# Kernel optimization log

Hardware: AMD Instinct MI355X
Metric: run time of the kernel (lower is better)

## Reference

```python
import jax, jax.numpy as jnp
import numpy as np

B, S, D = 2, 2048, 4096
H, KVH, HD = 32, 8, 128          # n_heads, n_kv_heads, head_dim
N_REP = H // KVH                 # GQA repeat factor
ROPE_THETA = 10000.0
NEG = -1e9                       # finite stand-in for -inf additive mask


def setup_inputs() -> dict:
    key = jax.random.key(0)
    ks = jax.random.split(key, 5)
    x = jax.random.normal(ks[0], (B, S, D), jnp.float32)
    wq = jax.random.normal(ks[1], (D, H * HD), jnp.float32) * 0.02
    wk = jax.random.normal(ks[2], (D, KVH * HD), jnp.float32) * 0.02
    wv = jax.random.normal(ks[3], (D, KVH * HD), jnp.float32) * 0.02
    wo = jax.random.normal(ks[4], (D, D), jnp.float32) * 0.02
    # rotary frequencies: freq_cis[t, j] = exp(i * t * theta^(-2j/HD))
    inv_freq = 1.0 / (ROPE_THETA ** (jnp.arange(0, HD, 2, dtype=jnp.float32) / HD))
    angles = jnp.arange(S, dtype=jnp.float32)[:, None] * inv_freq[None, :]  # [S, HD/2]
    cos, sin = jnp.cos(angles), jnp.sin(angles)
    # causal additive mask [S, S]
    i = jnp.arange(S)
    mask = jnp.where(i[None, :] > i[:, None], NEG, 0.0).astype(jnp.float32)
    return {"x": x, "cos": cos, "sin": sin, "mask": mask,
            "wq": wq, "wk": wk, "wv": wv, "wo": wo, "start_pos": 0}


def _apply_rope(t, cos, sin):
    # t: [B, S, nH, HD] -> rotate consecutive pairs, matching view_as_complex semantics
    tp = t.reshape(*t.shape[:-1], HD // 2, 2)
    t0, t1 = tp[..., 0], tp[..., 1]
    c = cos[None, :, None, :]  # [1, S, 1, HD/2]
    s = sin[None, :, None, :]
    o0 = t0 * c - t1 * s
    o1 = t0 * s + t1 * c
    return jnp.stack([o0, o1], axis=-1).reshape(t.shape)


def reference(x, cos, sin, mask, wq, wk, wv, wo, start_pos):
    bs, seq_len, _ = x.shape
    q = (x @ wq).reshape(bs, seq_len, H, HD)
    k = (x @ wk).reshape(bs, seq_len, KVH, HD)
    v = (x @ wv).reshape(bs, seq_len, KVH, HD)
    q = _apply_rope(q, cos, sin)
    k = _apply_rope(k, cos, sin)
    # start_pos == 0 full prefill: KV cache slice [:, :start_pos+seq_len] == k, v
    # GQA: repeat_interleave kv heads (each kv head repeated N_REP times consecutively)
    k = jnp.repeat(k, N_REP, axis=2)  # [B, S, H, HD]
    v = jnp.repeat(v, N_REP, axis=2)
    attn = jnp.einsum('bqhd,bkhd->bhqk', q, k) / jnp.sqrt(jnp.float32(HD))
    attn = attn + mask[None, None, :, :]
    p = jax.nn.softmax(attn.astype(jnp.float32), axis=-1).astype(q.dtype)
    out = jnp.einsum('bhqk,bkhd->bqhd', p, v).reshape(bs, seq_len, D)
    return out @ wo
```

## Files before the change

kernel.cpp:

```cpp
#include <hip/hip_runtime.h>
#include <stdint.h>

typedef unsigned short u16;
typedef __attribute__((ext_vector_type(8))) short bf16x8;
typedef __attribute__((ext_vector_type(4))) float f32x4;

__device__ __forceinline__ u16 f2bf(float f) {
  uint32_t x = __float_as_uint(f);
  x += 0x7fffu + ((x >> 16) & 1u);
  return (u16)(x >> 16);
}
__device__ __forceinline__ float bf2f(u16 u) {
  return __uint_as_float(((uint32_t)u) << 16);
}
__device__ __forceinline__ void gload_lds16(const void* g, void* l) {
  __builtin_amdgcn_global_load_lds(
      (const __attribute__((address_space(1))) void*)g,
      (__attribute__((address_space(3))) void*)l, 16, 0, 0);
}

__device__ __forceinline__ float rope_rot(float a, int col, int srow,
                                          const float* __restrict__ cosT,
                                          const float* __restrict__ sinT) {
  float p = __shfl_xor(a, 1, 64);
  int d = (col & 127) >> 1;
  float c = cosT[srow * 64 + d];
  float sn = sinT[srow * 64 + d];
  return (col & 1) ? (p * sn + a * c) : (a * c - p * sn);
}

__global__ __launch_bounds__(256) void cvt_kernel(const float* __restrict__ x,
                                                  u16* __restrict__ y) {
  int i = blockIdx.x * 256 + threadIdx.x;
  float4 v = ((const float4*)x)[i];
  ushort4 o = make_ushort4(f2bf(v.x), f2bf(v.y), f2bf(v.z), f2bf(v.w));
  ((ushort4*)y)[i] = o;
}

__global__ __launch_bounds__(256) void transpose_cvt(const float* __restrict__ W,
                                                     u16* __restrict__ Wt,
                                                     int Kd, int Nd) {
  __shared__ float t[32][33];
  int k0 = blockIdx.y * 32, n0 = blockIdx.x * 32;
  int tx = threadIdx.x, ty = threadIdx.y;
  #pragma unroll
  for (int i = ty; i < 32; i += 8)
    t[i][tx] = W[(size_t)(k0 + i) * Nd + n0 + tx];
  __syncthreads();
  #pragma unroll
  for (int i = ty; i < 32; i += 8)
    Wt[(size_t)(n0 + i) * Kd + k0 + tx] = f2bf(t[tx][i]);
}

__global__ __launch_bounds__(256) void gemm_kv(const u16* __restrict__ A,
                                               const u16* __restrict__ Bt,
                                               u16* __restrict__ Kout,
                                               u16* __restrict__ Vt,
                                               const float* __restrict__ cosT,
                                               const float* __restrict__ sinT) {
  const int K = 4096;
  __shared__ __attribute__((aligned(16))) u16 sA[128 * 64];
  __shared__ __attribute__((aligned(16))) u16 sB[128 * 64];
  const int tid = threadIdx.x;
  const int wave = tid >> 6, lane = tid & 63;
  const int lr = lane & 15, lq = lane >> 4;
  const int bm = blockIdx.y * 128, bn = blockIdx.x * 128;
  const int wm = (wave >> 1) * 64, wn = (wave & 1) * 64;
  f32x4 acc[4][4] = {};
  for (int kt = 0; kt < K; kt += 64) {
    #pragma unroll
    for (int c = 0; c < 4; ++c) {
      int chunk = wave * 4 + c;
      int eo = chunk * 512 + lane * 8;
      int r = eo >> 6, col = eo & 63;
      gload_lds16(A + (size_t)(bm + r) * K + kt + col, sA + chunk * 512);
      gload_lds16(Bt + (size_t)(bn + r) * K + kt + col, sB + chunk * 512);
    }
    __syncthreads();
    #pragma unroll
    for (int ks = 0; ks < 2; ++ks) {
      bf16x8 af[4], bfv[4];
      #pragma unroll
      for (int i = 0; i < 4; ++i)
        af[i] = *(const bf16x8*)(sA + (wm + i * 16 + lr) * 64 + ks * 32 + lq * 8);
      #pragma unroll
      for (int j = 0; j < 4; ++j)
        bfv[j] = *(const bf16x8*)(sB + (wn + j * 16 + lr) * 64 + ks * 32 + lq * 8);
      #pragma unroll
      for (int i = 0; i < 4; ++i)
        #pragma unroll
        for (int j = 0; j < 4; ++j)
          acc[i][j] = __builtin_amdgcn_mfma_f32_16x16x32_bf16(af[i], bfv[j], acc[i][j], 0, 0, 0);
    }
    __syncthreads();
  }
  #pragma unroll
  for (int i = 0; i < 4; ++i) {
    #pragma unroll
    for (int j = 0; j < 4; ++j) {
      int colg = bn + wn + j * 16 + lr;
      if (bn < 1024) {
        #pragma unroll
        for (int r = 0; r < 4; ++r) {
          int row = bm + wm + i * 16 + lq * 4 + r;
          float o = rope_rot(acc[i][j][r], colg, row & 2047, cosT, sinT);
          Kout[(size_t)row * 1024 + colg] = f2bf(o);
        }
      } else {
        int col = colg - 1024;
        int row0 = bm + wm + i * 16 + lq * 4;
        int bb = row0 >> 11, s = row0 & 2047;
        ushort4 pk = make_ushort4(f2bf(acc[i][j][0]), f2bf(acc[i][j][1]),
                                  f2bf(acc[i][j][2]), f2bf(acc[i][j][3]));
        *(ushort4*)(Vt + ((size_t)bb * 1024 + col) * 2048 + s) = pk;
      }
    }
  }
}

template <int EPI, bool ROPE>
__global__ __launch_bounds__(512, 2) void gemm256(const u16* __restrict__ A,
                                                  const u16* __restrict__ Bt,
                                                  void* __restrict__ Cout,
                                                  int M, int N, int K,
                                                  const float* __restrict__ cosT,
                                                  const float* __restrict__ sinT,
                                                  float post) {
  __shared__ __attribute__((aligned(16))) u16 sA[2][256 * 64];
  __shared__ __attribute__((aligned(16))) u16 sB[2][256 * 64];
  const int tid = threadIdx.x;
  const int wid = tid >> 6, lane = tid & 63;
  const int lr = lane & 15, lq = lane >> 4;
  const int bm = blockIdx.y * 256, bn = blockIdx.x * 256;
  const int wrow = (wid >> 2) * 128, wcol = (wid & 3) * 64;
  const int NK = K >> 6;

  f32x4 acc[8][4] = {};

  auto stageA = [&](int j) {
    u16* dst = &sA[j & 1][0];
    #pragma unroll
    for (int c = 0; c < 4; ++c) {
      int e = (c * 512 + tid) * 8;
      int r = e >> 6, col = e & 63;
      gload_lds16(A + (size_t)(bm + r) * K + j * 64 + (col ^ ((r & 7) << 3)), dst + e);
    }
  };
  auto stageB = [&](int j) {
    u16* dst = &sB[j & 1][0];
    #pragma unroll
    for (int c = 0; c < 4; ++c) {
      int e = (c * 512 + tid) * 8;
      int r = e >> 6, col = e & 63;
      gload_lds16(Bt + (size_t)(bn + r) * K + j * 64 + (col ^ ((r & 7) << 3)), dst + e);
    }
  };

  stageB(0); stageA(0); stageB(1);
  asm volatile("s_waitcnt vmcnt(4)" ::: "memory");
  asm volatile("s_barrier" ::: "memory");

  for (int j = 0; j < NK; ++j) {
    const u16* a_ = sA[j & 1];
    const u16* b_ = sB[j & 1];
    #pragma unroll
    for (int ks = 0; ks < 2; ++ks) {
      bf16x8 af[8], bf[4];
      #pragma unroll
      for (int mf = 0; mf < 8; ++mf) {
        int row = wrow + mf * 16 + lr;
        af[mf] = *(const bf16x8*)(a_ + row * 64 + ((ks * 32 + lq * 8) ^ ((row & 7) << 3)));
      }
      #pragma unroll
      for (int nf = 0; nf < 4; ++nf) {
        int row = wcol + nf * 16 + lr;
        bf[nf] = *(const bf16x8*)(b_ + row * 64 + ((ks * 32 + lq * 8) ^ ((row & 7) << 3)));
      }
      if (ks == 0) {
        if (j + 1 < NK) stageA(j + 1);
      }
      asm volatile("s_barrier" ::: "memory");
      if (ks == 1 && j + 2 < NK) stageB(j + 2);
      __builtin_amdgcn_s_setprio(1);
      #pragma unroll
      for (int mf = 0; mf < 8; ++mf)
        #pragma unroll
        for (int nf = 0; nf < 4; ++nf)
          acc[mf][nf] = __builtin_amdgcn_mfma_f32_16x16x32_bf16(af[mf], bf[nf],
                                                                acc[mf][nf], 0, 0, 0);
      __builtin_amdgcn_s_setprio(0);
      if (ks == 1) {
        if (j < NK - 2)       asm volatile("s_waitcnt vmcnt(4)" ::: "memory");
        else if (j == NK - 2) asm volatile("s_waitcnt vmcnt(0)" ::: "memory");
      }
      asm volatile("s_barrier" ::: "memory");
    }
  }

  #pragma unroll
  for (int mf = 0; mf < 8; ++mf) {
    #pragma unroll
    for (int nf = 0; nf < 4; ++nf) {
      #pragma unroll
      for (int r = 0; r < 4; ++r) {
        int row = bm + wrow + mf * 16 + lq * 4 + r;
        int col = bn + wcol + nf * 16 + lr;
        if (ROPE) {
          float o = rope_rot(acc[mf][nf][r], col, row & 2047, cosT, sinT);
          ((u16*)Cout)[(size_t)row * N + col] = f2bf(o * post);
        } else if (EPI == 0) {
          ((u16*)Cout)[(size_t)row * N + col] = f2bf(acc[mf][nf][r]);
        } else {
          ((float*)Cout)[(size_t)row * N + col] = acc[mf][nf][r];
        }
      }
    }
  }
}

__global__ __launch_bounds__(256, 2) void attn_kernel(const u16* __restrict__ Q,
                                                      const u16* __restrict__ Kb,
                                                      const u16* __restrict__ Vt,
                                                      u16* __restrict__ O) {
  __shared__ __attribute__((aligned(16))) u16 sK[2][64 * 128];
  __shared__ __attribute__((aligned(16))) u16 sV[2][128 * 64];
  __shared__ __attribute__((aligned(16))) u16 sP[4][16 * 66];
  const int tid = threadIdx.x;
  const int wave = tid >> 6, lane = tid & 63;
  const int lr = lane & 15, lq = lane >> 4;
  const int p = blockIdx.x & 15;
  const int h = (blockIdx.x >> 4) & 31;
  const int b = blockIdx.x >> 9;
  const int kvh = h >> 2;
  const int qtA = p, qtB = 31 - p;
  const int q0A = qtA * 64 + wave * 16;
  const int q0B = qtB * 64 + wave * 16;
  const float NOFF = -8.0f;

  bf16x8 qfA[4], qfB[4];
  {
    const u16* qa = Q + (size_t)(b * 2048 + q0A + lr) * 4096 + h * 128 + lq * 8;
    const u16* qb = Q + (size_t)(b * 2048 + q0B + lr) * 4096 + h * 128 + lq * 8;
    #pragma unroll
    for (int ks = 0; ks < 4; ++ks) {
      qfA[ks] = *(const bf16x8*)(qa + ks * 32);
      qfB[ks] = *(const bf16x8*)(qb + ks * 32);
    }
  }

  const u16* kbase = Kb + (size_t)b * 2048 * 1024 + kvh * 128;
  const u16* vbase = Vt + (size_t)(b * 1024 + kvh * 128) * 2048;

  auto stage = [&](int kt, int bsel) {
    #pragma unroll
    for (int c = 0; c < 4; ++c) {
      int chunk = wave * 4 + c;
      int eo = chunk * 512 + lane * 8;
      int rk = eo >> 7, ck = eo & 127;
      int cks = ck ^ ((rk & 7) << 3);
      gload_lds16(kbase + (size_t)(kt * 64 + rk) * 1024 + cks,
                  (u16*)sK[bsel] + chunk * 512);
      int rv = eo >> 6, cv = eo & 63;
      int cvs = cv ^ ((rv & 7) << 3);
      gload_lds16(vbase + (size_t)rv * 2048 + kt * 64 + cvs,
                  (u16*)sV[bsel] + chunk * 512);
    }
  };

  f32x4 oA[8] = {}, oB[8] = {};
  float lA[4] = {0.f, 0.f, 0.f, 0.f}, lB[4] = {0.f, 0.f, 0.f, 0.f};

  stage(0, 0);
  __syncthreads();
  int buf = 0;
  for (int kt = 0; kt <= qtB; ++kt) {
    if (kt < qtB) stage(kt + 1, buf ^ 1);
    const u16* kb_ = sK[buf];
    const u16* vb_ = sV[buf];
    const bool doA = (kt <= qtA);

    f32x4 sAacc[4], sBacc[4];
    #pragma unroll
    for (int nf = 0; nf < 4; ++nf) {
      sAacc[nf] = (f32x4){NOFF, NOFF, NOFF, NOFF};
      sBacc[nf] = (f32x4){NOFF, NOFF, NOFF, NOFF};
    }
    __builtin_amdgcn_s_setprio(1);
    #pragma unroll
    for (int ks = 0; ks < 4; ++ks) {
      bf16x8 kf[4];
      #pragma unroll
      for (int nf = 0; nf < 4; ++nf) {
        int row = nf * 16 + lr;
        kf[nf] = *(const bf16x8*)(kb_ + row * 128 + ((ks * 32 + lq * 8) ^ ((row & 7) << 3)));
      }
      #pragma unroll
      for (int nf = 0; nf < 4; ++nf)
        sBacc[nf] = __builtin_amdgcn_mfma_f32_16x16x32_bf16(qfB[ks], kf[nf], sBacc[nf], 0, 0, 0);
      if (doA) {
        #pragma unroll
        for (int nf = 0; nf < 4; ++nf)
          sAacc[nf] = __builtin_amdgcn_mfma_f32_16x16x32_bf16(qfA[ks], kf[nf], sAacc[nf], 0, 0, 0);
      }
    }
    __builtin_amdgcn_s_setprio(0);

    auto sm_pv = [&](f32x4* sacc, float* lsum, f32x4* o, int qt, int q0) {
      float ls[4] = {0.f, 0.f, 0.f, 0.f};
      const bool diag = (kt == qt);
      #pragma unroll
      for (int nf = 0; nf < 4; ++nf)
        #pragma unroll
        for (int r = 0; r < 4; ++r) {
          float pv = __expf(sacc[nf][r]);
          if (diag) {
            int j = kt * 64 + nf * 16 + lr;
            int iq = q0 + lq * 4 + r;
            if (j > iq) pv = 0.f;
          }
          ls[r] += pv;
          sP[wave][(lq * 4 + r) * 66 + nf * 16 + lr] = f2bf(pv);
        }
      #pragma unroll
      for (int r = 0; r < 4; ++r) lsum[r] += ls[r];
      __builtin_amdgcn_s_setprio(1);
      #pragma unroll
      for (int ks = 0; ks < 2; ++ks) {
        bf16x8 pa = *(const bf16x8*)(&sP[wave][lr * 66 + ks * 32 + lq * 8]);
        #pragma unroll
        for (int df = 0; df < 8; ++df) {
          int row = df * 16 + lr;
          bf16x8 vb = *(const bf16x8*)(vb_ + row * 64 + ((ks * 32 + lq * 8) ^ ((row & 7) << 3)));
          o[df] = __builtin_amdgcn_mfma_f32_16x16x32_bf16(pa, vb, o[df], 0, 0, 0);
        }
      }
      __builtin_amdgcn_s_setprio(0);
    };

    if (doA) sm_pv(sAacc, lA, oA, qtA, q0A);
    sm_pv(sBacc, lB, oB, qtB, q0B);

    __syncthreads();
    buf ^= 1;
  }

  #pragma unroll
  for (int r = 0; r < 4; ++r) {
    float tA = lA[r], tB = lB[r];
    tA += __shfl_xor(tA, 1, 64); tB += __shfl_xor(tB, 1, 64);
    tA += __shfl_xor(tA, 2, 64); tB += __shfl_xor(tB, 2, 64);
    tA += __shfl_xor(tA, 4, 64); tB += __shfl_xor(tB, 4, 64);
    tA += __shfl_xor(tA, 8, 64); tB += __shfl_xor(tB, 8, 64);
    lA[r] = 1.f / tA; lB[r] = 1.f / tB;
  }
  #pragma unroll
  for (int df = 0; df < 8; ++df) {
    #pragma unroll
    for (int r = 0; r < 4; ++r) {
      int iqA = q0A + lq * 4 + r;
      int iqB = q0B + lq * 4 + r;
      O[(size_t)(b * 2048 + iqA) * 4096 + h * 128 + df * 16 + lr] = f2bf(oA[df][r] * lA[r]);
      O[(size_t)(b * 2048 + iqB) * 4096 + h * 128 + df * 16 + lr] = f2bf(oB[df][r] * lB[r]);
    }
  }
}

extern "C" void kernel_launch(void* const* d_in, const int* in_sizes, int n_in,
                              void* d_out, int out_size, void* d_ws, size_t ws_size,
                              hipStream_t stream) {
  (void)in_sizes; (void)n_in; (void)out_size;
  const float* x    = (const float*)d_in[0];
  const float* cosT = (const float*)d_in[1];
  const float* sinT = (const float*)d_in[2];
  const float* wq   = (const float*)d_in[4];
  const float* wk   = (const float*)d_in[5];
  const float* wv   = (const float*)d_in[6];
  const float* wo   = (const float*)d_in[7];
  float* out = (float*)d_out;
  char* ws = (char*)d_ws;

  const size_t WS_NEEDED = 201326592;
  if (ws_size < WS_NEEDED) return;

  u16* xb   = (u16*)(ws);
  u16* wqt  = (u16*)(ws + 33554432ULL);
  u16* wkvt = (u16*)(ws + 67108864ULL);
  u16* wot  = (u16*)(ws + 83886080ULL);
  u16* Qb   = (u16*)(ws + 117440512ULL);
  u16* Kbf  = (u16*)(ws + 150994944ULL);
  u16* Vt   = (u16*)(ws + 159383552ULL);
  u16* Ob   = (u16*)(ws + 167772160ULL);

  const float QSC = 0.08838834764831845f;

  cvt_kernel<<<16384, 256, 0, stream>>>(x, xb);
  transpose_cvt<<<dim3(128, 128), dim3(32, 8), 0, stream>>>(wq, wqt, 4096, 4096);
  transpose_cvt<<<dim3(32, 128),  dim3(32, 8), 0, stream>>>(wk, wkvt, 4096, 1024);
  transpose_cvt<<<dim3(32, 128),  dim3(32, 8), 0, stream>>>(wv, wkvt + 1024ULL * 4096, 4096, 1024);
  transpose_cvt<<<dim3(128, 128), dim3(32, 8), 0, stream>>>(wo, wot, 4096, 4096);

  gemm256<0, true><<<dim3(16, 16), 512, 0, stream>>>(xb, wqt, Qb, 4096, 4096, 4096,
                                                     cosT, sinT, QSC);
  gemm_kv<<<dim3(16, 32), 256, 0, stream>>>(xb, wkvt, Kbf, Vt, cosT, sinT);

  attn_kernel<<<1024, 256, 0, stream>>>(Qb, Kbf, Vt, Ob);

  gemm256<2, false><<<dim3(16, 16), 512, 0, stream>>>(Ob, wot, out, 4096, 4096, 4096,
                                                      nullptr, nullptr, 1.0f);
}
```

Measured before the change: 536.9 us.

## Split GEMM mainloop into four phases interleaving half-tile loads with MFMA

Restructures the 256x256 GEMM main loop into four sub-phases per K step. Each phase loads only a quarter of the A fragments and issues half of an A or B tile prefetch, so global-to-LDS traffic is spread evenly across compute and register pressure drops. It also remaps block indices with an XCD-aware swizzle so neighbouring tiles land on the same chiplet for L2 reuse. In exchange there are more barriers per iteration, and the swizzle assumes the block count divides by 8.

```diff
diff --git a/kernel.cpp b/kernel.cpp
--- a/kernel.cpp
+++ b/kernel.cpp
@@ -131,67 +131,88 @@
   const int tid = threadIdx.x;
   const int wid = tid >> 6, lane = tid & 63;
   const int lr = lane & 15, lq = lane >> 4;
-  const int bm = blockIdx.y * 256, bn = blockIdx.x * 256;
+  const int nbn = N >> 8;
+  int lin = blockIdx.y * gridDim.x + blockIdx.x;
+  int cpx = (gridDim.x * gridDim.y) >> 3;
+  int swz = (lin & 7) * cpx + (lin >> 3);
+  const int bm = (swz / nbn) * 256, bn = (swz % nbn) * 256;
   const int wrow = (wid >> 2) * 128, wcol = (wid & 3) * 64;
   const int NK = K >> 6;
 
   f32x4 acc[8][4] = {};
 
-  auto stageA = [&](int j) {
-    u16* dst = &sA[j & 1][0];
-    #pragma unroll
-    for (int c = 0; c < 4; ++c) {
+  auto stageAh = [&](int j, int h) {
+    u16* dst = &sA[j & 1][h * 8192];
+    #pragma unroll
+    for (int c = 0; c < 2; ++c) {
       int e = (c * 512 + tid) * 8;
       int r = e >> 6, col = e & 63;
-      gload_lds16(A + (size_t)(bm + r) * K + j * 64 + (col ^ ((r & 7) << 3)), dst + e);
+      gload_lds16(A + (size_t)(bm + h * 128 + r) * K + j * 64 + (col ^ ((r & 7) << 3)),
+                  dst + e);
     }
   };
-  auto stageB = [&](int j) {
-    u16* dst = &sB[j & 1][0];
-    #pragma unroll
-    for (int c = 0; c < 4; ++c) {
+  auto stageBh = [&](int j, int h) {
+    u16* dst = &sB[j & 1][h * 8192];
+    #pragma unroll
+    for (int c = 0; c < 2; ++c) {
       int e = (c * 512 + tid) * 8;
       int r = e >> 6, col = e & 63;
-      gload_lds16(Bt + (size_t)(bn + r) * K + j * 64 + (col ^ ((r & 7) << 3)), dst + e);
+      gload_lds16(Bt + (size_t)(bn + h * 128 + r) * K + j * 64 + (col ^ ((r & 7) << 3)),
+                  dst + e);
     }
   };
 
-  stageB(0); stageA(0); stageB(1);
+  stageBh(0, 0); stageBh(0, 1);
+  stageAh(0, 0); stageAh(0, 1);
+  stageBh(1, 0); stageBh(1, 1);
   asm volatile("s_waitcnt vmcnt(4)" ::: "memory");
   asm volatile("s_barrier" ::: "memory");
 
   for (int j = 0; j < NK; ++j) {
     const u16* a_ = sA[j & 1];
     const u16* b_ = sB[j & 1];
-    #pragma unroll
-    for (int ks = 0; ks < 2; ++ks) {
-      bf16x8 af[8], bf[4];
-      #pragma unroll
-      for (int mf = 0; mf < 8; ++mf) {
-        int row = wrow + mf * 16 + lr;
-        af[mf] = *(const bf16x8*)(a_ + row * 64 + ((ks * 32 + lq * 8) ^ ((row & 7) << 3)));
-      }
-      #pragma unroll
-      for (int nf = 0; nf < 4; ++nf) {
-        int row = wcol + nf * 16 + lr;
-        bf[nf] = *(const bf16x8*)(b_ + row * 64 + ((ks * 32 + lq * 8) ^ ((row & 7) << 3)));
-      }
-      if (ks == 0) {
-        if (j + 1 < NK) stageA(j + 1);
-      }
+    bf16x8 bfr[4][2];
+    #pragma unroll
+    for (int q = 0; q < 4; ++q) {
+      if (q == 0) {
+        #pragma unroll
+        for (int nf = 0; nf < 4; ++nf) {
+          int row = wcol + nf * 16 + lr;
+          #pragma unroll
+          for (int ks = 0; ks < 2; ++ks)
+            bfr[nf][ks] = *(const bf16x8*)(b_ + row * 64 +
+                              ((ks * 32 + lq * 8) ^ ((row & 7) << 3)));
+        }
+      }
+      bf16x8 af[2][2];
+      #pragma unroll
+      for (int mf = 0; mf < 2; ++mf) {
+        int row = wrow + q * 32 + mf * 16 + lr;
+        #pragma unroll
+        for (int ks = 0; ks < 2; ++ks)
+          af[mf][ks] = *(const bf16x8*)(a_ + row * 64 +
+                            ((ks * 32 + lq * 8) ^ ((row & 7) << 3)));
+      }
+      if (q == 0)      { if (j + 1 < NK) stageAh(j + 1, 0); }
+      else if (q == 1) { if (j + 1 < NK) stageAh(j + 1, 1); }
+      else if (q == 2) { if (j + 2 < NK) stageBh(j + 2, 0); }
+      else             { if (j + 2 < NK) stageBh(j + 2, 1); }
       asm volatile("s_barrier" ::: "memory");
-      if (ks == 1 && j + 2 < NK) stageB(j + 2);
+      asm volatile("s_waitcnt lgkmcnt(0)" ::: "memory");
+      __builtin_amdgcn_sched_barrier(0);
       __builtin_amdgcn_s_setprio(1);
       #pragma unroll
-      for (int mf = 0; mf < 8; ++mf)
-        #pragma unroll
-        for (int nf = 0; nf < 4; ++nf)
-          acc[mf][nf] = __builtin_amdgcn_mfma_f32_16x16x32_bf16(af[mf], bf[nf],
-                                                                acc[mf][nf], 0, 0, 0);
+      for (int ks = 0; ks < 2; ++ks)
+        #pragma unroll
+        for (int mf = 0; mf < 2; ++mf)
+          #pragma unroll
+          for (int nf = 0; nf < 4; ++nf)
+            acc[q * 2 + mf][nf] = __builtin_amdgcn_mfma_f32_16x16x32_bf16(
+                af[mf][ks], bfr[nf][ks], acc[q * 2 + mf][nf], 0, 0, 0);
       __builtin_amdgcn_s_setprio(0);
-      if (ks == 1) {
-        if (j < NK - 2)       asm volatile("s_waitcnt vmcnt(4)" ::: "memory");
-        else if (j == NK - 2) asm volatile("s_waitcnt vmcnt(0)" ::: "memory");
+      if (q == 3) {
+        if (j + 2 < NK)      asm volatile("s_waitcnt vmcnt(4)" ::: "memory");
+        else if (j + 1 < NK) asm volatile("s_waitcnt vmcnt(0)" ::: "memory");
       }
       asm volatile("s_barrier" ::: "memory");
     }
```

Result: no change. 544.5 us (+1.4%).

## Double-buffer LDS fragment reads in GEMM loop to overlap with MFMA

Applied to the files above, without the earlier changes.

Restructures the GEMM main loop so the LDS-to-register fragment reads for the next k-substep are issued before the current substep's MFMAs. Two register sets (P/Q) ping-pong between the halves of each k-tile. Partial lgkmcnt waits and sched_barriers pin the ordering so MFMAs run while LDS reads are in flight. The goal is to hide LDS read latency and drop one barrier per half-step. The cost is more register pressure from the extra fragment set, and the vmcnt(0) wait every iteration may expose global load latency.

```diff
diff --git a/kernel.cpp b/kernel.cpp
--- a/kernel.cpp
+++ b/kernel.cpp
@@ -155,46 +155,59 @@
       gload_lds16(Bt + (size_t)(bn + r) * K + j * 64 + (col ^ ((r & 7) << 3)), dst + e);
     }
   };
+  auto readA = [&](bf16x8* af, const u16* a_, int ks) {
+    #pragma unroll
+    for (int mf = 0; mf < 8; ++mf) {
+      int row = wrow + mf * 16 + lr;
+      af[mf] = *(const bf16x8*)(a_ + row * 64 + ((ks * 32 + lq * 8) ^ ((row & 7) << 3)));
+    }
+  };
+  auto readB = [&](bf16x8* bfv, const u16* b_, int ks) {
+    #pragma unroll
+    for (int nf = 0; nf < 4; ++nf) {
+      int row = wcol + nf * 16 + lr;
+      bfv[nf] = *(const bf16x8*)(b_ + row * 64 + ((ks * 32 + lq * 8) ^ ((row & 7) << 3)));
+    }
+  };
+
+  bf16x8 afP[8], bfP[4], afQ[8], bfQ[4];
 
   stageB(0); stageA(0); stageB(1);
   asm volatile("s_waitcnt vmcnt(4)" ::: "memory");
   asm volatile("s_barrier" ::: "memory");
+  readA(afP, sA[0], 0); readB(bfP, sB[0], 0);
 
   for (int j = 0; j < NK; ++j) {
     const u16* a_ = sA[j & 1];
     const u16* b_ = sB[j & 1];
-    #pragma unroll
-    for (int ks = 0; ks < 2; ++ks) {
-      bf16x8 af[8], bf[4];
-      #pragma unroll
-      for (int mf = 0; mf < 8; ++mf) {
-        int row = wrow + mf * 16 + lr;
-        af[mf] = *(const bf16x8*)(a_ + row * 64 + ((ks * 32 + lq * 8) ^ ((row & 7) << 3)));
-      }
-      #pragma unroll
-      for (int nf = 0; nf < 4; ++nf) {
-        int row = wcol + nf * 16 + lr;
-        bf[nf] = *(const bf16x8*)(b_ + row * 64 + ((ks * 32 + lq * 8) ^ ((row & 7) << 3)));
-      }
-      if (ks == 0) {
-        if (j + 1 < NK) stageA(j + 1);
-      }
-      asm volatile("s_barrier" ::: "memory");
-      if (ks == 1 && j + 2 < NK) stageB(j + 2);
-      __builtin_amdgcn_s_setprio(1);
-      #pragma unroll
-      for (int mf = 0; mf < 8; ++mf)
-        #pragma unroll
-        for (int nf = 0; nf < 4; ++nf)
-          acc[mf][nf] = __builtin_amdgcn_mfma_f32_16x16x32_bf16(af[mf], bf[nf],
-                                                                acc[mf][nf], 0, 0, 0);
-      __builtin_amdgcn_s_setprio(0);
-      if (ks == 1) {
-        if (j < NK - 2)       asm volatile("s_waitcnt vmcnt(4)" ::: "memory");
-        else if (j == NK - 2) asm volatile("s_waitcnt vmcnt(0)" ::: "memory");
-      }
-      asm volatile("s_barrier" ::: "memory");
-    }
+    const u16* an = sA[(j + 1) & 1];
+    const u16* bn = sB[(j + 1) & 1];
+    readA(afQ, a_, 1); readB(bfQ, b_, 1);
+    if (j + 1 < NK) stageA(j + 1);
+    asm volatile("s_waitcnt lgkmcnt(12)" ::: "memory");
+    __builtin_amdgcn_sched_barrier(0);
+    __builtin_amdgcn_s_setprio(1);
+    #pragma unroll
+    for (int mf = 0; mf < 8; ++mf)
+      #pragma unroll
+      for (int nf = 0; nf < 4; ++nf)
+        acc[mf][nf] = __builtin_amdgcn_mfma_f32_16x16x32_bf16(afP[mf], bfP[nf],
+                                                              acc[mf][nf], 0, 0, 0);
+    __builtin_amdgcn_s_setprio(0);
+    asm volatile("s_waitcnt vmcnt(0)" ::: "memory");
+    asm volatile("s_barrier" ::: "memory");
+    readA(afP, an, 0); readB(bfP, bn, 0);
+    if (j + 2 < NK) stageB(j + 2);
+    asm volatile("s_waitcnt lgkmcnt(12)" ::: "memory");
+    __builtin_amdgcn_sched_barrier(0);
+    __builtin_amdgcn_s_setprio(1);
+    #pragma unroll
+    for (int mf = 0; mf < 8; ++mf)
+      #pragma unroll
+      for (int nf = 0; nf < 4; ++nf)
+        acc[mf][nf] = __builtin_amdgcn_mfma_f32_16x16x32_bf16(afQ[mf], bfQ[nf],
+                                                              acc[mf][nf], 0, 0, 0);
+    __builtin_amdgcn_s_setprio(0);
   }
 
   #pragma unroll
```

Result: no change. 529.7 us (-1.3%).
